# Kernel tuning notes

Measured on AMD Instinct MI355X. Metric: run time of the kernel, lower is better.

## Reference

```python
import jax, jax.numpy as jnp
import numpy as np

EPS = 1e-5  # torch BatchNorm2d default eps


def _bn(t, gamma, beta, mean, var):
    # t: (N, S, C, T, V); params: (S, C) -- eval-mode batchnorm per subset
    g = gamma[None, :, :, None, None]
    b = beta[None, :, :, None, None]
    m = mean[None, :, :, None, None]
    v = var[None, :, :, None, None]
    return g * (t - m) * jax.lax.rsqrt(v + EPS) + b


def setup_inputs() -> dict:
    key = jax.random.key(0)
    ks = jax.random.split(key, 20)
    N, C, T, V = 64, 64, 300, 25
    S, OC, IC = 3, 64, 16  # subsets, out_channels, inter_channels (64 // 4)
    f32 = jnp.float32
    inp = {}
    inp['x'] = jax.random.normal(ks[0], (N, C, T, V), dtype=f32)
    inp['A'] = jax.random.uniform(ks[1], (S, V, V), dtype=f32) * 0.1
    inp['alpha'] = jnp.array([0.5], dtype=f32)
    sc_a = 1.0 / np.sqrt(C)
    inp['conv_a_w'] = jax.random.normal(ks[2], (S, IC, C), dtype=f32) * sc_a
    inp['conv_a_b'] = jax.random.normal(ks[3], (S, IC), dtype=f32) * 0.01
    inp['conv_b_w'] = jax.random.normal(ks[4], (S, IC, C), dtype=f32) * sc_a
    inp['conv_b_b'] = jax.random.normal(ks[5], (S, IC), dtype=f32) * 0.01
    inp['bn_a_gamma'] = jnp.ones((S, IC), dtype=f32)
    inp['bn_a_beta'] = jnp.zeros((S, IC), dtype=f32)
    inp['bn_a_mean'] = jax.random.normal(ks[6], (S, IC), dtype=f32) * 0.1
    inp['bn_a_var'] = jax.random.uniform(ks[7], (S, IC), dtype=f32) + 0.5
    inp['bn_b_gamma'] = jnp.ones((S, IC), dtype=f32)
    inp['bn_b_beta'] = jnp.zeros((S, IC), dtype=f32)
    inp['bn_b_mean'] = jax.random.normal(ks[8], (S, IC), dtype=f32) * 0.1
    inp['bn_b_var'] = jax.random.uniform(ks[9], (S, IC), dtype=f32) + 0.5
    inp['conv_d_w'] = jax.random.normal(ks[10], (S, OC, C), dtype=f32) * sc_a
    inp['conv_d_b'] = jax.random.normal(ks[11], (S, OC), dtype=f32) * 0.01
    inp['bn_gamma'] = jnp.ones((OC,), dtype=f32)
    inp['bn_beta'] = jnp.zeros((OC,), dtype=f32)
    inp['bn_mean'] = jax.random.normal(ks[12], (OC,), dtype=f32) * 0.1
    inp['bn_var'] = jax.random.uniform(ks[13], (OC,), dtype=f32) + 0.5
    return inp


def reference(x, A, alpha, conv_a_w, conv_a_b, conv_b_w, conv_b_b,
              bn_a_gamma, bn_a_beta, bn_a_mean, bn_a_var,
              bn_b_gamma, bn_b_beta, bn_b_mean, bn_b_var,
              conv_d_w, conv_d_b, bn_gamma, bn_beta, bn_mean, bn_var):
    # x: (N, C, T, V). All subsets computed in a single vectorized pass.
    # conv_a / conv_b are 1x1 convs == channel contractions.
    a = jnp.einsum('nctv,sic->nsitv', x, conv_a_w) + conv_a_b[None, :, :, None, None]
    b = jnp.einsum('nctv,sic->nsitv', x, conv_b_w) + conv_b_b[None, :, :, None, None]
    a = jnp.tanh(_bn(a, bn_a_gamma, bn_a_beta, bn_a_mean, bn_a_var))
    b = jnp.tanh(_bn(b, bn_b_gamma, bn_b_beta, bn_b_mean, bn_b_var))
    # adaptive adjacency: contract inter_c*T -> (N, S, V, V), normalize, tanh, scale
    denom = a.shape[2] * a.shape[3]  # inter_c * T
    M = jnp.einsum('nsitv,nsitw->nsvw', a, b) / denom
    A_adp = A[None, :, :, :] + jnp.tanh(M) * alpha[0]
    # graph conv: x.view(N, C*T, V) @ A1 per subset, then 1x1 conv_d, summed over subsets
    xm = jnp.einsum('nctv,nsvw->nsctw', x, A_adp)
    y = jnp.einsum('nsctw,soc->notw', xm, conv_d_w) + conv_d_b.sum(0)[None, :, None, None]
    # output BN + residual (in_c == out_c so down is identity) + relu
    y = (bn_gamma[None, :, None, None] * (y - bn_mean[None, :, None, None])
         * jax.lax.rsqrt(bn_var[None, :, None, None] + EPS)
         + bn_beta[None, :, None, None])
    return jax.nn.relu(y + x)
```

## Files before the change

### kernel.cpp

```cpp
#include <hip/hip_runtime.h>
#include <math.h>

typedef __attribute__((ext_vector_type(8))) short bf16x8;
typedef __attribute__((ext_vector_type(4))) float f32x4;
typedef __attribute__((ext_vector_type(4))) unsigned short us4;

__device__ inline unsigned short f2bf(float f) {
  union { float f; unsigned u; } v; v.f = f;
  return (unsigned short)((v.u + 0x7FFF + ((v.u >> 16) & 1)) >> 16);
}
__device__ inline float tanh_fast(float x) {
  return 1.0f - 2.0f * __builtin_amdgcn_rcpf(
                           __builtin_amdgcn_exp2f(x * 2.885390081777927f) + 1.0f);
}

__global__ __launch_bounds__(256) void k_xT(const float* __restrict__ x,
                                            unsigned short* __restrict__ xTg) {
  __shared__ float xt[125 * 65];
  const int tid = threadIdx.x, n = blockIdx.y, tb = blockIdx.x * 125;
  const float* xn = x + (size_t)n * 480000;
  for (int e = tid; e < 8000; e += 256) {
    int c = e / 125, i = e - c * 125;
    xt[i * 65 + c] = xn[(size_t)c * 7500 + tb + i];
  }
  __syncthreads();
  unsigned short* dst = xTg + ((size_t)n * 7500 + tb) * 64;
  for (int e = tid; e < 8000; e += 256) {
    int i = e >> 6, c = e & 63;
    dst[(size_t)i * 64 + c] = f2bf(xt[i * 65 + c]);
  }
}

__global__ __launch_bounds__(256) void k_M(
    const unsigned short* __restrict__ xTg,
    const float* __restrict__ wa, const float* __restrict__ wab,
    const float* __restrict__ wb, const float* __restrict__ wbb,
    const float* __restrict__ ga, const float* __restrict__ bea,
    const float* __restrict__ ma, const float* __restrict__ va,
    const float* __restrict__ gb, const float* __restrict__ beb,
    const float* __restrict__ mb, const float* __restrict__ vb,
    float* __restrict__ Mbuf) {
  __shared__ unsigned short ab2[2][32 * 256];
  const int tid = threadIdx.x, lane = tid & 63;
  const int wid = tid >> 6;
  const int s = blockIdx.x, bx = blockIdx.y, n = blockIdx.z;
  const int l15 = lane & 15, lg = lane >> 4;

  for (int e = tid; e < 4096; e += 256) ((unsigned long long*)ab2)[e] = 0ull;

  bf16x8 afrag[2][2];
#pragma unroll
  for (int rt = 0; rt < 2; ++rt) {
    const float* W = (rt ? wb : wa) + ((size_t)s * 16 + l15) * 64;
#pragma unroll
    for (int Ks = 0; Ks < 2; ++Ks) {
      const float* p = W + Ks * 32 + lg * 8;
      bf16x8 f;
#pragma unroll
      for (int j = 0; j < 8; ++j) f[j] = (short)f2bf(p[j]);
      afrag[rt][Ks] = f;
    }
  }

  float scv[2][4], shv[2][4];
#pragma unroll
  for (int r = 0; r < 4; ++r) {
    int i = s * 16 + lg * 4 + r;
    float sc = ga[i] * rsqrtf(va[i] + 1e-5f);
    scv[0][r] = sc; shv[0][r] = (wab[i] - ma[i]) * sc + bea[i];
    sc = gb[i] * rsqrtf(vb[i] + 1e-5f);
    scv[1][r] = sc; shv[1][r] = (wbb[i] - mb[i]) * sc + beb[i];
  }

  const int vt = wid >> 1, wt = wid & 1;
  f32x4 facc = {0.f, 0.f, 0.f, 0.f};
  const unsigned short* xbase = xTg + (size_t)n * 7500 * 64;

  for (int chunk = 0; chunk < 4; ++chunk) {
    const int tvb = (bx * 4 + chunk) * 375;
    __syncthreads();
#pragma unroll
    for (int ct = 0; ct < 6; ++ct) {
      int col = (wid * 6 + ct) * 16 + l15;
      bool valid = col < 375;
      int colc = valid ? col : 374;
      const unsigned short* bp = xbase + (size_t)(tvb + colc) * 64 + lg * 8;
      bf16x8 bf0 = *(const bf16x8*)bp;
      bf16x8 bf1 = *(const bf16x8*)(bp + 32);
      int tl = colc / 25, v = colc - tl * 25;
      int kp = tl * 16 + lg * 4;
#pragma unroll
      for (int rt = 0; rt < 2; ++rt) {
        f32x4 d = {0.f, 0.f, 0.f, 0.f};
        d = __builtin_amdgcn_mfma_f32_16x16x32_bf16(afrag[rt][0], bf0, d, 0, 0, 0);
        d = __builtin_amdgcn_mfma_f32_16x16x32_bf16(afrag[rt][1], bf1, d, 0, 0, 0);
        if (valid) {
          us4 pk;
#pragma unroll
          for (int r = 0; r < 4; ++r)
            pk[r] = f2bf(tanh_fast(d[r] * scv[rt][r] + shv[rt][r]));
          unsigned byte = ((unsigned)(v * 256 + kp) * 2) ^ ((v & 7) << 4);
          *(us4*)((char*)ab2[rt] + byte) = pk;
        }
      }
    }
    __syncthreads();
#pragma unroll
    for (int ks = 0; ks < 8; ++ks) {
      int va_ = vt * 16 + l15, wa_ = wt * 16 + l15;
      unsigned ab_ = ((unsigned)(va_ * 256 + lg * 8 + ks * 32) * 2) ^ ((va_ & 7) << 4);
      unsigned bb_ = ((unsigned)(wa_ * 256 + lg * 8 + ks * 32) * 2) ^ ((wa_ & 7) << 4);
      bf16x8 af = *(bf16x8*)((char*)ab2[0] + ab_);
      bf16x8 bf = *(bf16x8*)((char*)ab2[1] + bb_);
      facc = __builtin_amdgcn_mfma_f32_16x16x32_bf16(af, bf, facc, 0, 0, 0);
    }
  }
  const int w = wt * 16 + l15;
  if (w < 25) {
    float* Mrow = Mbuf + ((size_t)n * 3 + s) * 625;
#pragma unroll
    for (int r = 0; r < 4; ++r) {
      int v = vt * 16 + lg * 4 + r;
      if (v < 25) atomicAdd(Mrow + v * 25 + w, facc[r]);
    }
  }
}

__global__ __launch_bounds__(256) void k_adp(const float* __restrict__ Mbuf,
                                             const float* __restrict__ A,
                                             const float* __restrict__ alpha,
                                             float* __restrict__ Aadp) {
  int idx = blockIdx.x * 256 + threadIdx.x;
  if (idx < 120000) {
    int vw = idx % 625;
    int s = (idx / 625) % 3;
    Aadp[idx] = A[s * 625 + vw] + tanh_fast(Mbuf[idx] * (1.0f / 4800.0f)) * alpha[0];
  }
}

__global__ __launch_bounds__(256) void k_y(
    const float* __restrict__ x, const float* __restrict__ Aadp,
    const float* __restrict__ wd, const float* __restrict__ db,
    const float* __restrict__ bng, const float* __restrict__ bnb,
    const float* __restrict__ bnm, const float* __restrict__ bnv,
    float* __restrict__ out) {
  __shared__ unsigned short xmT[256 * 64];
  __shared__ unsigned short AaT[3][32 * 40];
  const int tid = threadIdx.x, lane = tid & 63, wid = tid >> 6;
  const int l15 = lane & 15, lg = lane >> 4;
  const int bx = blockIdx.x, n = blockIdx.y;
  const int t0 = bx * 10;

  for (int e = tid; e < 3 * 32 * 40 / 4; e += 256) ((unsigned long long*)AaT)[e] = 0ull;
  __syncthreads();
  const float* Aan = Aadp + (size_t)n * 1875;
  for (int e = tid; e < 1875; e += 256) {
    int s = e / 625, r = e - s * 625, v = r / 25, w = r - v * 25;
    AaT[s][w * 40 + v] = f2bf(Aan[e]);
  }

  float sc4[4], sh4[4];
#pragma unroll
  for (int r = 0; r < 4; ++r) {
    int o = wid * 16 + lg * 4 + r;
    float sc = bng[o] * rsqrtf(bnv[o] + 1e-5f);
    sc4[r] = sc;
    sh4[r] = (db[o] + db[64 + o] + db[128 + o] - bnm[o]) * sc + bnb[o];
  }

  const float* xn = x + (size_t)n * 480000;
  bf16x8 xfrag[10];
  {
    const int c = wid * 16 + l15;
    const float* xr = xn + (size_t)c * 7500 + t0 * 25;
#pragma unroll
    for (int t = 0; t < 10; ++t) {
      bf16x8 f;
#pragma unroll
      for (int j = 0; j < 8; ++j) {
        int v = lg * 8 + j;
        f[j] = (v < 25) ? (short)f2bf(xr[t * 25 + v]) : (short)0;
      }
      xfrag[t] = f;
    }
  }
  __syncthreads();

  f32x4 yacc[16];
#pragma unroll
  for (int i = 0; i < 16; ++i) yacc[i] = (f32x4){0.f, 0.f, 0.f, 0.f};

  for (int s = 0; s < 3; ++s) {
    bf16x8 af0 = *(bf16x8*)(&AaT[s][l15 * 40 + lg * 8]);
    bf16x8 af1 = *(bf16x8*)(&AaT[s][(16 + l15) * 40 + lg * 8]);
    const int c = wid * 16 + l15;
#pragma unroll
    for (int t = 0; t < 10; ++t) {
#pragma unroll
      for (int wt = 0; wt < 2; ++wt) {
        f32x4 d = {0.f, 0.f, 0.f, 0.f};
        d = __builtin_amdgcn_mfma_f32_16x16x32_bf16(wt ? af1 : af0, xfrag[t], d, 0, 0, 0);
#pragma unroll
        for (int r = 0; r < 4; ++r) {
          int w = wt * 16 + lg * 4 + r;
          if (w < 25) {
            int tw = t * 25 + w;
            unsigned byte = ((unsigned)(tw * 64 + c) * 2) ^ ((tw & 7) << 4);
            *(unsigned short*)((char*)xmT + byte) = f2bf(d[r]);
          }
        }
      }
    }
    __syncthreads();
    bf16x8 wf0, wf1;
    {
      const float* wp = wd + ((size_t)s * 64 + wid * 16 + l15) * 64 + lg * 8;
#pragma unroll
      for (int j = 0; j < 8; ++j) {
        wf0[j] = (short)f2bf(wp[j]);
        wf1[j] = (short)f2bf(wp[32 + j]);
      }
    }
#pragma unroll
    for (int ct = 0; ct < 16; ++ct) {
      int tw = ct * 16 + l15;
      unsigned b0 = ((unsigned)(tw * 64 + lg * 8) * 2) ^ ((tw & 7) << 4);
      unsigned b1 = ((unsigned)(tw * 64 + 32 + lg * 8) * 2) ^ ((tw & 7) << 4);
      bf16x8 xb0 = *(bf16x8*)((char*)xmT + b0);
      bf16x8 xb1 = *(bf16x8*)((char*)xmT + b1);
      yacc[ct] = __builtin_amdgcn_mfma_f32_16x16x32_bf16(wf0, xb0, yacc[ct], 0, 0, 0);
      yacc[ct] = __builtin_amdgcn_mfma_f32_16x16x32_bf16(wf1, xb1, yacc[ct], 0, 0, 0);
    }
    __syncthreads();
  }

  float* outn = out + (size_t)n * 480000;
#pragma unroll
  for (int ct = 0; ct < 16; ++ct) {
    int tw = ct * 16 + l15;
    if (tw < 250) {
      int t = tw / 25, w = tw - t * 25;
      size_t base = (size_t)(t0 + t) * 25 + w;
#pragma unroll
      for (int r = 0; r < 4; ++r) {
        int o = wid * 16 + lg * 4 + r;
        size_t addr = (size_t)o * 7500 + base;
        float val = yacc[ct][r] * sc4[r] + sh4[r] + xn[addr];
        outn[addr] = fmaxf(val, 0.f);
      }
    }
  }
}

extern "C" void kernel_launch(void* const* d_in, const int* in_sizes, int n_in,
                              void* d_out, int out_size, void* d_ws,
                              size_t ws_size, hipStream_t stream) {
  const float* x = (const float*)d_in[0];
  const float* A = (const float*)d_in[1];
  const float* alpha = (const float*)d_in[2];
  const float* wa = (const float*)d_in[3];
  const float* wab = (const float*)d_in[4];
  const float* wb = (const float*)d_in[5];
  const float* wbb = (const float*)d_in[6];
  const float* ga = (const float*)d_in[7];
  const float* bea = (const float*)d_in[8];
  const float* ma = (const float*)d_in[9];
  const float* va = (const float*)d_in[10];
  const float* gb = (const float*)d_in[11];
  const float* beb = (const float*)d_in[12];
  const float* mb = (const float*)d_in[13];
  const float* vb = (const float*)d_in[14];
  const float* wd = (const float*)d_in[15];
  const float* db = (const float*)d_in[16];
  const float* bng = (const float*)d_in[17];
  const float* bnb = (const float*)d_in[18];
  const float* bnm = (const float*)d_in[19];
  const float* bnv = (const float*)d_in[20];

  float* ws = (float*)d_ws;
  float* Mbuf = ws;
  float* Aadp = ws + 120000;
  unsigned short* xTg = (unsigned short*)d_out;

  hipMemsetAsync(Mbuf, 0, 120000 * sizeof(float), stream);
  k_xT<<<dim3(60, 64), 256, 0, stream>>>(x, xTg);
  k_M<<<dim3(3, 5, 64), 256, 0, stream>>>(xTg, wa, wab, wb, wbb, ga, bea, ma,
                                          va, gb, beb, mb, vb, Mbuf);
  k_adp<<<469, 256, 0, stream>>>(Mbuf, A, alpha, Aadp);
  k_y<<<dim3(30, 64), 256, 0, stream>>>(x, Aadp, wd, db, bng, bnb, bnm, bnv,
                                        (float*)d_out);
}
```

Before: 480.2 us.

## Restructure M and y kernels: shared x tile across subsets, bf16 adjacency and weights

k_M now handles all three subsets in one block. It stages a 250-column x tile in shared memory once and reuses it for every subset, where before each subset block read x separately from global memory. k_adp writes the adaptive adjacency as a padded, transposed bf16 array that k_y loads straight into MFMA fragments, and a new prep kernel converts conv_d weights to bf16 once. k_y uses smaller time tiles staged through swizzled shared memory and takes the residual from the bf16 shared copy instead of rereading x in fp32. This lowers residual precision and adds a kernel launch in exchange.

```diff
diff --git a/kernel.cpp b/kernel.cpp
--- a/kernel.cpp
+++ b/kernel.cpp
@@ -9,9 +9,19 @@
   union { float f; unsigned u; } v; v.f = f;
   return (unsigned short)((v.u + 0x7FFF + ((v.u >> 16) & 1)) >> 16);
 }
+__device__ inline float bf2f(unsigned short b) {
+  union { unsigned u; float f; } v; v.u = ((unsigned)b) << 16;
+  return v.f;
+}
 __device__ inline float tanh_fast(float x) {
   return 1.0f - 2.0f * __builtin_amdgcn_rcpf(
                            __builtin_amdgcn_exp2f(x * 2.885390081777927f) + 1.0f);
+}
+
+__global__ __launch_bounds__(256) void k_prep(const float* __restrict__ wd,
+                                              unsigned short* __restrict__ wdb) {
+  int idx = blockIdx.x * 256 + threadIdx.x;
+  if (idx < 12288) wdb[idx] = f2bf(wd[idx]);
 }
 
 __global__ __launch_bounds__(256) void k_xT(const float* __restrict__ x,
@@ -40,88 +50,102 @@
     const float* __restrict__ gb, const float* __restrict__ beb,
     const float* __restrict__ mb, const float* __restrict__ vb,
     float* __restrict__ Mbuf) {
-  __shared__ unsigned short ab2[2][32 * 256];
-  const int tid = threadIdx.x, lane = tid & 63;
-  const int wid = tid >> 6;
-  const int s = blockIdx.x, bx = blockIdx.y, n = blockIdx.z;
+  __shared__ unsigned short xt[250 * 64];
+  __shared__ unsigned short ab2[2][32 * 192];
+
+  const int tid = threadIdx.x, lane = tid & 63, wid = tid >> 6;
   const int l15 = lane & 15, lg = lane >> 4;
-
-  for (int e = tid; e < 4096; e += 256) ((unsigned long long*)ab2)[e] = 0ull;
-
-  bf16x8 afrag[2][2];
-#pragma unroll
-  for (int rt = 0; rt < 2; ++rt) {
-    const float* W = (rt ? wb : wa) + ((size_t)s * 16 + l15) * 64;
-#pragma unroll
-    for (int Ks = 0; Ks < 2; ++Ks) {
-      const float* p = W + Ks * 32 + lg * 8;
-      bf16x8 f;
-#pragma unroll
-      for (int j = 0; j < 8; ++j) f[j] = (short)f2bf(p[j]);
-      afrag[rt][Ks] = f;
-    }
-  }
-
-  float scv[2][4], shv[2][4];
-#pragma unroll
-  for (int r = 0; r < 4; ++r) {
-    int i = s * 16 + lg * 4 + r;
-    float sc = ga[i] * rsqrtf(va[i] + 1e-5f);
-    scv[0][r] = sc; shv[0][r] = (wab[i] - ma[i]) * sc + bea[i];
-    sc = gb[i] * rsqrtf(vb[i] + 1e-5f);
-    scv[1][r] = sc; shv[1][r] = (wbb[i] - mb[i]) * sc + beb[i];
-  }
+  const int bx = blockIdx.x, n = blockIdx.y;
+
+  for (int e = tid; e < 3072; e += 256) ((unsigned long long*)ab2)[e] = 0ull;
+
+  bf16x8 afrag[3][2][2];
+#pragma unroll
+  for (int s = 0; s < 3; ++s)
+#pragma unroll
+    for (int rt = 0; rt < 2; ++rt) {
+      const float* W = (rt ? wb : wa) + ((size_t)s * 16 + l15) * 64;
+#pragma unroll
+      for (int Ks = 0; Ks < 2; ++Ks) {
+        bf16x8 f;
+        const float* p = W + Ks * 32 + lg * 8;
+#pragma unroll
+        for (int j = 0; j < 8; ++j) f[j] = (short)f2bf(p[j]);
+        afrag[s][rt][Ks] = f;
+      }
+    }
+  float scv[3][2][4], shv[3][2][4];
+#pragma unroll
+  for (int s = 0; s < 3; ++s)
+#pragma unroll
+    for (int r = 0; r < 4; ++r) {
+      int i = s * 16 + lg * 4 + r;
+      float sc = ga[i] * rsqrtf(va[i] + 1e-5f);
+      scv[s][0][r] = sc; shv[s][0][r] = (wab[i] - ma[i]) * sc + bea[i];
+      sc = gb[i] * rsqrtf(vb[i] + 1e-5f);
+      scv[s][1][r] = sc; shv[s][1][r] = (wbb[i] - mb[i]) * sc + beb[i];
+    }
 
   const int vt = wid >> 1, wt = wid & 1;
-  f32x4 facc = {0.f, 0.f, 0.f, 0.f};
-  const unsigned short* xbase = xTg + (size_t)n * 7500 * 64;
-
-  for (int chunk = 0; chunk < 4; ++chunk) {
-    const int tvb = (bx * 4 + chunk) * 375;
+  f32x4 facc[3];
+#pragma unroll
+  for (int s = 0; s < 3; ++s) facc[s] = (f32x4){0.f, 0.f, 0.f, 0.f};
+  const unsigned short* xbase = xTg + (size_t)n * 480000;
+
+  for (int chunk = 0; chunk < 3; ++chunk) {
+    const int tvb = (bx * 3 + chunk) * 250;
     __syncthreads();
-#pragma unroll
-    for (int ct = 0; ct < 6; ++ct) {
-      int col = (wid * 6 + ct) * 16 + l15;
-      bool valid = col < 375;
-      int colc = valid ? col : 374;
-      const unsigned short* bp = xbase + (size_t)(tvb + colc) * 64 + lg * 8;
-      bf16x8 bf0 = *(const bf16x8*)bp;
-      bf16x8 bf1 = *(const bf16x8*)(bp + 32);
-      int tl = colc / 25, v = colc - tl * 25;
-      int kp = tl * 16 + lg * 4;
-#pragma unroll
-      for (int rt = 0; rt < 2; ++rt) {
-        f32x4 d = {0.f, 0.f, 0.f, 0.f};
-        d = __builtin_amdgcn_mfma_f32_16x16x32_bf16(afrag[rt][0], bf0, d, 0, 0, 0);
-        d = __builtin_amdgcn_mfma_f32_16x16x32_bf16(afrag[rt][1], bf1, d, 0, 0, 0);
-        if (valid) {
-          us4 pk;
-#pragma unroll
-          for (int r = 0; r < 4; ++r)
-            pk[r] = f2bf(tanh_fast(d[r] * scv[rt][r] + shv[rt][r]));
-          unsigned byte = ((unsigned)(v * 256 + kp) * 2) ^ ((v & 7) << 4);
-          *(us4*)((char*)ab2[rt] + byte) = pk;
+    for (int u = tid; u < 2000; u += 256) {
+      int tv = u >> 3, q = u & 7;
+      bf16x8 val = *(const bf16x8*)(xbase + (size_t)(tvb + tv) * 64 + q * 8);
+      *(bf16x8*)((char*)xt + ((tv * 128 + q * 16) ^ ((tv & 7) << 4))) = val;
+    }
+    __syncthreads();
+#pragma unroll
+    for (int s = 0; s < 3; ++s) {
+#pragma unroll
+      for (int ct = 0; ct < 4; ++ct) {
+        int col = (wid * 4 + ct) * 16 + l15;
+        int colc = (col < 250) ? col : 249;
+        bf16x8 bf0 = *(bf16x8*)((char*)xt + ((colc * 128 + lg * 16) ^ ((colc & 7) << 4)));
+        bf16x8 bf1 = *(bf16x8*)((char*)xt + ((colc * 128 + 64 + lg * 16) ^ ((colc & 7) << 4)));
+        int tl = (colc * 41) >> 10, v = colc - tl * 25;
+        int kp = tl * 16 + lg * 4;
+#pragma unroll
+        for (int rt = 0; rt < 2; ++rt) {
+          f32x4 d = {0.f, 0.f, 0.f, 0.f};
+          d = __builtin_amdgcn_mfma_f32_16x16x32_bf16(afrag[s][rt][0], bf0, d, 0, 0, 0);
+          d = __builtin_amdgcn_mfma_f32_16x16x32_bf16(afrag[s][rt][1], bf1, d, 0, 0, 0);
+          if (col < 250) {
+            us4 pk;
+#pragma unroll
+            for (int r = 0; r < 4; ++r)
+              pk[r] = f2bf(tanh_fast(d[r] * scv[s][rt][r] + shv[s][rt][r]));
+            *(us4*)((char*)ab2[rt] + ((v * 384 + kp * 2) ^ ((v & 7) << 4))) = pk;
+          }
         }
       }
-    }
-    __syncthreads();
-#pragma unroll
-    for (int ks = 0; ks < 8; ++ks) {
-      int va_ = vt * 16 + l15, wa_ = wt * 16 + l15;
-      unsigned ab_ = ((unsigned)(va_ * 256 + lg * 8 + ks * 32) * 2) ^ ((va_ & 7) << 4);
-      unsigned bb_ = ((unsigned)(wa_ * 256 + lg * 8 + ks * 32) * 2) ^ ((wa_ & 7) << 4);
-      bf16x8 af = *(bf16x8*)((char*)ab2[0] + ab_);
-      bf16x8 bf = *(bf16x8*)((char*)ab2[1] + bb_);
-      facc = __builtin_amdgcn_mfma_f32_16x16x32_bf16(af, bf, facc, 0, 0, 0);
+      __syncthreads();
+#pragma unroll
+      for (int ks = 0; ks < 6; ++ks) {
+        int va_ = vt * 16 + l15, wa_ = wt * 16 + l15;
+        bf16x8 af = *(bf16x8*)((char*)ab2[0] + ((va_ * 384 + ks * 64 + lg * 16) ^ ((va_ & 7) << 4)));
+        bf16x8 bf = *(bf16x8*)((char*)ab2[1] + ((wa_ * 384 + ks * 64 + lg * 16) ^ ((wa_ & 7) << 4)));
+        facc[s] = __builtin_amdgcn_mfma_f32_16x16x32_bf16(af, bf, facc[s], 0, 0, 0);
+      }
+      __syncthreads();
     }
   }
   const int w = wt * 16 + l15;
   if (w < 25) {
-    float* Mrow = Mbuf + ((size_t)n * 3 + s) * 625;
-#pragma unroll
-    for (int r = 0; r < 4; ++r) {
-      int v = vt * 16 + lg * 4 + r;
-      if (v < 25) atomicAdd(Mrow + v * 25 + w, facc[r]);
+#pragma unroll
+    for (int s = 0; s < 3; ++s) {
+      float* Mrow = Mbuf + ((size_t)n * 3 + s) * 625;
+#pragma unroll
+      for (int r = 0; r < 4; ++r) {
+        int v = vt * 16 + lg * 4 + r;
+        if (v < 25) atomicAdd(Mrow + v * 25 + w, facc[s][r]);
+      }
     }
   }
 }
@@ -129,34 +153,42 @@
 __global__ __launch_bounds__(256) void k_adp(const float* __restrict__ Mbuf,
                                              const float* __restrict__ A,
                                              const float* __restrict__ alpha,
-                                             float* __restrict__ Aadp) {
+                                             unsigned short* __restrict__ AadpT) {
   int idx = blockIdx.x * 256 + threadIdx.x;
-  if (idx < 120000) {
-    int vw = idx % 625;
-    int s = (idx / 625) % 3;
-    Aadp[idx] = A[s * 625 + vw] + tanh_fast(Mbuf[idx] * (1.0f / 4800.0f)) * alpha[0];
+  if (idx < 196608) {
+    int v = idx & 31, w = (idx >> 5) & 31, ns = idx >> 10;
+    int s = ns % 3;
+    float val = 0.f;
+    if (v < 25 && w < 25)
+      val = A[s * 625 + v * 25 + w] +
+            tanh_fast(Mbuf[(size_t)ns * 625 + v * 25 + w] * (1.0f / 4800.0f)) * alpha[0];
+    AadpT[idx] = f2bf(val);
   }
 }
 
 __global__ __launch_bounds__(256) void k_y(
-    const float* __restrict__ x, const float* __restrict__ Aadp,
-    const float* __restrict__ wd, const float* __restrict__ db,
+    const float* __restrict__ x, const unsigned short* __restrict__ AadpT,
+    const unsigned short* __restrict__ wdb, const float* __restrict__ db,
     const float* __restrict__ bng, const float* __restrict__ bnb,
     const float* __restrict__ bnm, const float* __restrict__ bnv,
     float* __restrict__ out) {
-  __shared__ unsigned short xmT[256 * 64];
-  __shared__ unsigned short AaT[3][32 * 40];
+  __shared__ unsigned short xc[64 * 160];
+  __shared__ unsigned short xmT[128 * 64];
   const int tid = threadIdx.x, lane = tid & 63, wid = tid >> 6;
   const int l15 = lane & 15, lg = lane >> 4;
   const int bx = blockIdx.x, n = blockIdx.y;
-  const int t0 = bx * 10;
-
-  for (int e = tid; e < 3 * 32 * 40 / 4; e += 256) ((unsigned long long*)AaT)[e] = 0ull;
+  const int t0 = bx * 5;
+
+  for (int e = tid; e < 2560; e += 256) ((unsigned long long*)xc)[e] = 0ull;
   __syncthreads();
-  const float* Aan = Aadp + (size_t)n * 1875;
-  for (int e = tid; e < 1875; e += 256) {
-    int s = e / 625, r = e - s * 625, v = r / 25, w = r - v * 25;
-    AaT[s][w * 40 + v] = f2bf(Aan[e]);
+  const float* xn = x + (size_t)n * 480000;
+  for (int idx = tid; idx < 8192; idx += 256) {
+    int c = idx >> 7, j = idx & 127;
+    if (j < 125) {
+      int t = (j * 41) >> 10, v = j - t * 25;
+      unsigned short bv = f2bf(xn[(size_t)c * 7500 + t0 * 25 + j]);
+      *(unsigned short*)((char*)xc + ((c * 320 + t * 64 + v * 2) ^ ((c & 7) << 4))) = bv;
+    }
   }
 
   float sc4[4], sh4[4];
@@ -167,67 +199,47 @@
     sc4[r] = sc;
     sh4[r] = (db[o] + db[64 + o] + db[128 + o] - bnm[o]) * sc + bnb[o];
   }
-
-  const float* xn = x + (size_t)n * 480000;
-  bf16x8 xfrag[10];
-  {
-    const int c = wid * 16 + l15;
-    const float* xr = xn + (size_t)c * 7500 + t0 * 25;
-#pragma unroll
-    for (int t = 0; t < 10; ++t) {
-      bf16x8 f;
-#pragma unroll
-      for (int j = 0; j < 8; ++j) {
-        int v = lg * 8 + j;
-        f[j] = (v < 25) ? (short)f2bf(xr[t * 25 + v]) : (short)0;
-      }
-      xfrag[t] = f;
-    }
-  }
   __syncthreads();
 
-  f32x4 yacc[16];
-#pragma unroll
-  for (int i = 0; i < 16; ++i) yacc[i] = (f32x4){0.f, 0.f, 0.f, 0.f};
+  bf16x8 xf[5];
+#pragma unroll
+  for (int t = 0; t < 5; ++t)
+    xf[t] = *(bf16x8*)((char*)xc +
+                       (((wid * 16 + l15) * 320 + t * 64 + lg * 16) ^ ((l15 & 7) << 4)));
+
+  f32x4 yacc[8];
+#pragma unroll
+  for (int i = 0; i < 8; ++i) yacc[i] = (f32x4){0.f, 0.f, 0.f, 0.f};
 
   for (int s = 0; s < 3; ++s) {
-    bf16x8 af0 = *(bf16x8*)(&AaT[s][l15 * 40 + lg * 8]);
-    bf16x8 af1 = *(bf16x8*)(&AaT[s][(16 + l15) * 40 + lg * 8]);
-    const int c = wid * 16 + l15;
-#pragma unroll
-    for (int t = 0; t < 10; ++t) {
+    const unsigned short* Ab = AadpT + (((size_t)n * 3 + s) << 10);
+    bf16x8 bA0 = *(const bf16x8*)(Ab + l15 * 32 + lg * 8);
+    bf16x8 bA1 = *(const bf16x8*)(Ab + (16 + l15) * 32 + lg * 8);
+#pragma unroll
+    for (int t = 0; t < 5; ++t) {
 #pragma unroll
       for (int wt = 0; wt < 2; ++wt) {
         f32x4 d = {0.f, 0.f, 0.f, 0.f};
-        d = __builtin_amdgcn_mfma_f32_16x16x32_bf16(wt ? af1 : af0, xfrag[t], d, 0, 0, 0);
-#pragma unroll
-        for (int r = 0; r < 4; ++r) {
-          int w = wt * 16 + lg * 4 + r;
-          if (w < 25) {
-            int tw = t * 25 + w;
-            unsigned byte = ((unsigned)(tw * 64 + c) * 2) ^ ((tw & 7) << 4);
-            *(unsigned short*)((char*)xmT + byte) = f2bf(d[r]);
-          }
+        d = __builtin_amdgcn_mfma_f32_16x16x32_bf16(xf[t], wt ? bA1 : bA0, d, 0, 0, 0);
+        int w = wt * 16 + l15;
+        if (w < 25) {
+          int tw = t * 25 + w;
+          us4 pk;
+#pragma unroll
+          for (int r = 0; r < 4; ++r) pk[r] = f2bf(d[r]);
+          *(us4*)((char*)xmT + ((tw * 128 + wid * 32 + lg * 8) ^ ((tw & 7) << 4))) = pk;
         }
       }
     }
     __syncthreads();
-    bf16x8 wf0, wf1;
-    {
-      const float* wp = wd + ((size_t)s * 64 + wid * 16 + l15) * 64 + lg * 8;
-#pragma unroll
-      for (int j = 0; j < 8; ++j) {
-        wf0[j] = (short)f2bf(wp[j]);
-        wf1[j] = (short)f2bf(wp[32 + j]);
-      }
-    }
-#pragma unroll
-    for (int ct = 0; ct < 16; ++ct) {
+    const unsigned short* wp = wdb + ((size_t)s * 64 + wid * 16 + l15) * 64;
+    bf16x8 wf0 = *(const bf16x8*)(wp + lg * 8);
+    bf16x8 wf1 = *(const bf16x8*)(wp + 32 + lg * 8);
+#pragma unroll
+    for (int ct = 0; ct < 8; ++ct) {
       int tw = ct * 16 + l15;
-      unsigned b0 = ((unsigned)(tw * 64 + lg * 8) * 2) ^ ((tw & 7) << 4);
-      unsigned b1 = ((unsigned)(tw * 64 + 32 + lg * 8) * 2) ^ ((tw & 7) << 4);
-      bf16x8 xb0 = *(bf16x8*)((char*)xmT + b0);
-      bf16x8 xb1 = *(bf16x8*)((char*)xmT + b1);
+      bf16x8 xb0 = *(bf16x8*)((char*)xmT + ((tw * 128 + lg * 16) ^ ((tw & 7) << 4)));
+      bf16x8 xb1 = *(bf16x8*)((char*)xmT + ((tw * 128 + 64 + lg * 16) ^ ((tw & 7) << 4)));
       yacc[ct] = __builtin_amdgcn_mfma_f32_16x16x32_bf16(wf0, xb0, yacc[ct], 0, 0, 0);
       yacc[ct] = __builtin_amdgcn_mfma_f32_16x16x32_bf16(wf1, xb1, yacc[ct], 0, 0, 0);
     }
@@ -236,17 +248,17 @@
 
   float* outn = out + (size_t)n * 480000;
 #pragma unroll
-  for (int ct = 0; ct < 16; ++ct) {
+  for (int ct = 0; ct < 8; ++ct) {
     int tw = ct * 16 + l15;
-    if (tw < 250) {
-      int t = tw / 25, w = tw - t * 25;
-      size_t base = (size_t)(t0 + t) * 25 + w;
+    if (tw < 125) {
+      int t = (tw * 41) >> 10, w = tw - t * 25;
 #pragma unroll
       for (int r = 0; r < 4; ++r) {
         int o = wid * 16 + lg * 4 + r;
-        size_t addr = (size_t)o * 7500 + base;
-        float val = yacc[ct][r] * sc4[r] + sh4[r] + xn[addr];
-        outn[addr] = fmaxf(val, 0.f);
+        float res = bf2f(*(unsigned short*)(
+            (char*)xc + ((o * 320 + t * 64 + w * 2) ^ ((o & 7) << 4))));
+        float val = yacc[ct][r] * sc4[r] + sh4[r] + res;
+        outn[(size_t)o * 7500 + (size_t)(t0 + t) * 25 + w] = fmaxf(val, 0.f);
       }
     }
   }
@@ -277,16 +289,18 @@
   const float* bnm = (const float*)d_in[19];
   const float* bnv = (const float*)d_in[20];
 
-  float* ws = (float*)d_ws;
-  float* Mbuf = ws;
-  float* Aadp = ws + 120000;
+  char* ws = (char*)d_ws;
+  float* Mbuf = (float*)ws;
+  unsigned short* AadpT = (unsigned short*)(ws + 480000);
+  unsigned short* wdb = (unsigned short*)(ws + 873216);
   unsigned short* xTg = (unsigned short*)d_out;
 
-  hipMemsetAsync(Mbuf, 0, 120000 * sizeof(float), stream);
+  hipMemsetAsync(Mbuf, 0, 480000, stream);
+  k_prep<<<48, 256, 0, stream>>>(wd, wdb);
   k_xT<<<dim3(60, 64), 256, 0, stream>>>(x, xTg);
-  k_M<<<dim3(3, 5, 64), 256, 0, stream>>>(xTg, wa, wab, wb, wbb, ga, bea, ma,
-                                          va, gb, beb, mb, vb, Mbuf);
-  k_adp<<<469, 256, 0, stream>>>(Mbuf, A, alpha, Aadp);
-  k_y<<<dim3(30, 64), 256, 0, stream>>>(x, Aadp, wd, db, bng, bnb, bnm, bnv,
+  k_M<<<dim3(10, 64), 256, 0, stream>>>(xTg, wa, wab, wb, wbb, ga, bea, ma, va,
+                                        gb, beb, mb, vb, Mbuf);
+  k_adp<<<768, 256, 0, stream>>>(Mbuf, A, alpha, AadpT);
+  k_y<<<dim3(60, 64), 256, 0, stream>>>(x, AadpT, wdb, db, bng, bnb, bnm, bnv,
                                         (float*)d_out);
 }
```

Result: faster. 411.2 us (-14.4%).
